# Performance work log

Hardware: AMD Instinct MI355X
Metric: run time of the kernel (lower is better)

## Reference

```python
import jax, jax.numpy as jnp
import numpy as np

J, C, F, K = 4096, 8192, 64, 2  # jobs, total nodes, out feats, TAGConv hops (DGL default K=2)


def setup_inputs() -> dict:
    key = jax.random.key(0)
    ks = jax.random.split(key, 8)
    h = jax.random.uniform(ks[0], (J,), jnp.float32)
    L = jax.random.uniform(ks[1], (J,), jnp.float32)
    W = jax.random.uniform(ks[2], (), jnp.float32)
    P = jax.random.uniform(ks[3], (), jnp.float32)
    N = jax.random.uniform(ks[4], (), jnp.float32)
    Graph = jax.random.randint(ks[5], (J, C), 0, 2).astype(jnp.float32)
    tag_w = jax.random.normal(ks[6], ((K + 1) * 6, F), jnp.float32) * 0.05  # TAGConv lin weight on concat of K+1 hops
    tag_b = jnp.zeros((F,), jnp.float32)
    lin_w = jax.random.normal(ks[7], (F, C), jnp.float32) * 0.05
    lin_b = jnp.zeros((C,), jnp.float32)
    return dict(h=h, L=L, W=W, P=P, N=N, Graph=Graph,
                tag_w=tag_w, tag_b=tag_b, lin_w=lin_w, lin_b=lin_b)


def _mask(Graph):
    Jn, Cn = Graph.shape
    row = Graph.sum(axis=1, keepdims=True)          # [J,1]
    col = Graph.sum(axis=0, keepdims=True)          # [1,C]
    colJ = col[:, :Jn]                               # [1,J]
    left = 1.0 - row - row.T - colJ - colJ.T         # [J,J]
    left = jnp.where(left == 1.0, 1.0, 0.0)
    left = jnp.triu(left, k=1)
    right = 1.0 - jnp.broadcast_to(row, (Jn, Cn - Jn))
    return jnp.concatenate([left, right], axis=1)    # [J,C]


def reference(h, L, W, P, N, Graph, tag_w, tag_b, lin_w, lin_b):
    Jn, Cn = Graph.shape
    # sort jobs by h descending, pair with L
    order = jnp.argsort(-h)
    jobList = jnp.stack([h[order], L[order]], axis=1)                 # [J,2]
    other = jnp.stack([W, P, N, jnp.asarray(1.0, h.dtype)])           # [4]
    X = jnp.concatenate([jobList, jnp.broadcast_to(other, (Jn, 4))], axis=1)  # [J,6]
    X = jnp.concatenate([X, jnp.zeros((Cn - Jn, 6), X.dtype)], axis=0)        # [C,6]
    # pad adjacency to square CxC
    A = jnp.concatenate([Graph, jnp.zeros((Cn - Jn, Cn), Graph.dtype)], axis=0)
    # DGL TAGConv: norm = clamp(in_deg,1)^-0.5; edge i->j iff A[i,j]==1 => aggregate = A^T @ x
    deg = A.sum(axis=0)
    norm = jnp.clip(deg, 1.0) ** -0.5

    def prop(x):
        return (A.T @ (x * norm[:, None])) * norm[:, None]

    f0 = X
    f1 = prop(f0)
    f2 = prop(f1)
    G_t = jnp.concatenate([f0, f1, f2], axis=1) @ tag_w + tag_b       # [C,F]
    Value = G_t[:Jn] @ lin_w + lin_b                                   # [J,C]
    tmp = Value - (1.0 - _mask(Graph)) * 10000.0
    Poss = jax.nn.softmax(tmp.reshape(-1)).reshape(tmp.shape)
    return (Value, Poss)
```

## Files before the change

kernel.cpp:

```cpp
#include <hip/hip_runtime.h>
#include <math.h>

#define JN 4096
#define CN 8192

typedef __attribute__((ext_vector_type(8))) short short8;
typedef __attribute__((ext_vector_type(4))) float f32x4;

#define WS_LWT    0
#define WS_ROWSUM 262144
#define WS_DEG    266240
#define WS_NORM   270336
#define WS_X      274432
#define WS_F1     299008
#define WS_F2     323584
#define WS_PART   348160

#define PS_BITR    0
#define PS_COLPART 524288
#define PS_P1      589824
#define PS_P2      983040

__device__ __forceinline__ unsigned short f2bf(float x) {
    unsigned int u = __float_as_uint(x);
    u += 0x7fffu + ((u >> 16) & 1u);
    return (unsigned short)(u >> 16);
}

__device__ __forceinline__ float gt_val(const float* __restrict__ x, const float* __restrict__ a,
                                        const float* __restrict__ b, const float* __restrict__ tw,
                                        float acc, int f) {
#pragma unroll
    for (int k = 0; k < 6; ++k) acc += x[k] * tw[k * 64 + f];
#pragma unroll
    for (int k = 0; k < 6; ++k) acc += a[k] * tw[(k + 6) * 64 + f];
#pragma unroll
    for (int k = 0; k < 6; ++k) acc += b[k] * tw[(k + 12) * 64 + f];
    return acc;
}

__global__ __launch_bounds__(256) void k_front(const float* __restrict__ G,
                                               const float* __restrict__ h, const float* __restrict__ L,
                                               const float* __restrict__ Wp, const float* __restrict__ Pp,
                                               const float* __restrict__ Np,
                                               float* __restrict__ rowsum,
                                               unsigned long long* __restrict__ bitR,
                                               float* __restrict__ X) {
    __shared__ float redf[4];
    __shared__ int redi[4];
    int wv = threadIdx.x >> 6, lane = threadIdx.x & 63;
    if (blockIdx.x < JN) {
        int row = blockIdx.x;
        const f32x4* g4 = (const f32x4*)(G + (size_t)row * CN);
        unsigned long long* brow = bitR + (size_t)row * 64;
        float s = 0.f;
#pragma unroll
        for (int i = 0; i < 4; ++i) {
            f32x4 v = __builtin_nontemporal_load(&g4[i * 256 + wv * 64 + lane]);
            s += v[0] + v[1] + v[2] + v[3];
            unsigned long long b0 = __ballot(v[0] != 0.f);
            unsigned long long b1 = __ballot(v[1] != 0.f);
            unsigned long long b2 = __ballot(v[2] != 0.f);
            unsigned long long b3 = __ballot(v[3] != 0.f);
            if (!lane) {
                int base = i * 16 + wv * 4;
                brow[base] = b0; brow[base + 1] = b1; brow[base + 2] = b2; brow[base + 3] = b3;
            }
        }
#pragma unroll
        for (int i = 4; i < 8; ++i) {
            f32x4 v = __builtin_nontemporal_load(&g4[i * 256 + wv * 64 + lane]);
            s += v[0] + v[1] + v[2] + v[3];
        }
        for (int o = 32; o; o >>= 1) s += __shfl_down(s, o, 64);
        if (!lane) redf[wv] = s;
        __syncthreads();
        if (!threadIdx.x) rowsum[row] = redf[0] + redf[1] + redf[2] + redf[3];
    } else {
        int i = blockIdx.x - JN;
        float hi = h[i];
        int cnt = 0;
        for (int j = threadIdx.x; j < JN; j += 256) {
            float hj = h[j];
            cnt += (hj > hi) || (hj == hi && j < i);
        }
        for (int o = 32; o; o >>= 1) cnt += __shfl_down(cnt, o, 64);
        if (!lane) redi[wv] = cnt;
        __syncthreads();
        if (!threadIdx.x) {
            int r = redi[0] + redi[1] + redi[2] + redi[3];
            float* xr = X + r * 6;
            xr[0] = hi; xr[1] = L[i]; xr[2] = *Wp; xr[3] = *Pp; xr[4] = *Np; xr[5] = 1.f;
        }
    }
}

__global__ __launch_bounds__(256) void k_colsum_bits(const unsigned long long* __restrict__ bitR,
                                                     float* __restrict__ colpart) {
    __shared__ unsigned long long s_bits[256][4];
    int bx = blockIdx.x, r0 = blockIdx.y * 256;
    int tid = threadIdx.x;
    for (int t = tid; t < 1024; t += 256) {
        int r = t >> 2, wl = t & 3;
        s_bits[r][wl] = bitR[(size_t)(r0 + r) * 64 + bx * 4 + wl];
    }
    __syncthreads();
    int wl = tid & 3, bit = tid >> 2;
    int cnt = 0;
    for (int r = 0; r < 256; ++r)
        cnt += (int)((s_bits[r][wl] >> bit) & 1ull);
    colpart[(size_t)blockIdx.y * JN + bx * 256 + tid] = (float)cnt;
}

__global__ __launch_bounds__(256) void k_normred(const float* __restrict__ colpart,
                                                 float* __restrict__ deg, float* __restrict__ norm) {
    int j = blockIdx.x * 256 + threadIdx.x;
    float d = 0.f;
    for (int ch = 0; ch < 16; ++ch) d += colpart[(size_t)ch * JN + j];
    deg[j] = d;
    float dc = d < 1.f ? 1.f : d;
    norm[j] = rsqrtf(dc);
}

__global__ __launch_bounds__(256) void k_prop1(const unsigned long long* __restrict__ bitR,
                                               const float* __restrict__ X, const float* __restrict__ norm,
                                               float* __restrict__ part) {
    __shared__ unsigned long long s_bits[256][4];
    __shared__ float s_in[256 * 6];
    int bx = blockIdx.x, r0 = blockIdx.y * 256;
    int tid = threadIdx.x;
    for (int t = tid; t < 1024; t += 256) {
        int r = t >> 2, wl = t & 3;
        s_bits[r][wl] = bitR[(size_t)(r0 + r) * 64 + bx * 4 + wl];
    }
    for (int t = tid; t < 1536; t += 256) {
        int row = r0 + t / 6;
        s_in[t] = X[r0 * 6 + t] * norm[row];
    }
    __syncthreads();
    int wl = tid & 3, bit = tid >> 2;
    float a0 = 0, a1 = 0, a2 = 0, a3 = 0, a4 = 0, a5 = 0;
    for (int r = 0; r < 256; ++r) {
        float g = (float)((s_bits[r][wl] >> bit) & 1ull);
        const float* x = &s_in[r * 6];
        a0 += g * x[0]; a1 += g * x[1]; a2 += g * x[2];
        a3 += g * x[3]; a4 += g * x[4]; a5 += g * x[5];
    }
    float* o = part + ((size_t)blockIdx.y * JN + bx * 256 + tid) * 6;
    o[0] = a0; o[1] = a1; o[2] = a2; o[3] = a3; o[4] = a4; o[5] = a5;
}

__global__ __launch_bounds__(256) void k_prop2(const unsigned long long* __restrict__ bitR,
                                               const float* __restrict__ p1, const float* __restrict__ norm,
                                               float* __restrict__ f1, float* __restrict__ part) {
    __shared__ unsigned long long s_bits[256][4];
    __shared__ float s_in[256 * 6];
    int bx = blockIdx.x, r0 = blockIdx.y * 256;
    int tid = threadIdx.x;
    for (int t = tid; t < 1024; t += 256) {
        int r = t >> 2, wl = t & 3;
        s_bits[r][wl] = bitR[(size_t)(r0 + r) * 64 + bx * 4 + wl];
    }
    for (int t = tid; t < 1536; t += 256) {
        float s = 0.f;
        for (int ch = 0; ch < 16; ++ch) s += p1[(size_t)ch * 24576 + r0 * 6 + t];
        int row = r0 + t / 6;
        float n = norm[row];
        float f1v = s * n;
        if (bx == 0) f1[r0 * 6 + t] = f1v;
        s_in[t] = f1v * n;
    }
    __syncthreads();
    int wl = tid & 3, bit = tid >> 2;
    float a0 = 0, a1 = 0, a2 = 0, a3 = 0, a4 = 0, a5 = 0;
    for (int r = 0; r < 256; ++r) {
        float g = (float)((s_bits[r][wl] >> bit) & 1ull);
        const float* x = &s_in[r * 6];
        a0 += g * x[0]; a1 += g * x[1]; a2 += g * x[2];
        a3 += g * x[3]; a4 += g * x[4]; a5 += g * x[5];
    }
    float* o = part + ((size_t)blockIdx.y * JN + bx * 256 + tid) * 6;
    o[0] = a0; o[1] = a1; o[2] = a2; o[3] = a3; o[4] = a4; o[5] = a5;
}

__global__ __launch_bounds__(256) void k_fin2(const float* __restrict__ p2, const float* __restrict__ norm,
                                              float* __restrict__ f2) {
    int idx = blockIdx.x * 256 + threadIdx.x;
    float s = 0.f;
    for (int ch = 0; ch < 16; ++ch) s += p2[(size_t)ch * 24576 + idx];
    f2[idx] = s * norm[idx / 6];
}

__global__ __launch_bounds__(256) void k_lwT(const float* __restrict__ lw, unsigned short* __restrict__ lwT) {
    __shared__ float s[64][65];
    int c0 = blockIdx.x * 64;
    for (int t = threadIdx.x; t < 4096; t += 256) {
        int f = t >> 6, cc = t & 63;
        s[f][cc] = lw[(size_t)f * CN + c0 + cc];
    }
    __syncthreads();
    for (int q = threadIdx.x; q < 512; q += 256) {
        int c = q >> 3, kc = q & 7;
        short8 pack;
#pragma unroll
        for (int i = 0; i < 8; ++i) pack[i] = (short)f2bf(s[kc * 8 + i][c]);
        *(short8*)(lwT + ((size_t)(c0 + c)) * 64 + kc * 8) = pack;
    }
}

#define GEMM_PROLOGUE()                                                                   \
    __shared__ unsigned short sGt[64 * 64];                                               \
    __shared__ unsigned short sW[256 * 64];                                               \
    __shared__ float s_tw[18 * 64];                                                       \
    __shared__ float s_tb[64];                                                            \
    int j0 = blockIdx.y * 64, c0 = blockIdx.x * 256, tid = threadIdx.x;                   \
    for (int t = tid; t < 1152; t += 256) s_tw[t] = tw[t];                                \
    if (tid < 64) s_tb[tid] = tb[tid];                                                    \
    for (int q = tid; q < 2048; q += 256) {                                               \
        int col = q >> 3, off = q & 7;                                                    \
        short8 v = *(const short8*)(lwT + ((size_t)(c0 + col)) * 64 + off * 8);           \
        int byte = (col * 128 + off * 16) ^ ((col & 7) << 4);                             \
        *(short8*)((char*)sW + byte) = v;                                                 \
    }                                                                                     \
    __syncthreads();                                                                      \
    {                                                                                     \
        int row = tid & 63, fg = tid >> 6;                                                \
        const float* xr = X + (size_t)(j0 + row) * 6;                                     \
        const float* ar = f1 + (size_t)(j0 + row) * 6;                                    \
        const float* br = f2 + (size_t)(j0 + row) * 6;                                    \
        float xv[6], av[6], bv[6];                                                        \
        for (int k = 0; k < 6; ++k) { xv[k] = xr[k]; av[k] = ar[k]; bv[k] = br[k]; }      \
        short8 p0, p1v;                                                                   \
        for (int i = 0; i < 16; ++i) {                                                    \
            int f = fg * 16 + i;                                                          \
            float acc = gt_val(xv, av, bv, s_tw, s_tb[f], f);                             \
            unsigned short u = f2bf(acc);                                                 \
            if (i < 8) p0[i] = (short)u; else p1v[i - 8] = (short)u;                      \
        }                                                                                 \
        int base = row * 128 + fg * 32;                                                   \
        *(short8*)((char*)sGt + (base ^ ((row & 7) << 4))) = p0;                          \
        *(short8*)((char*)sGt + ((base + 16) ^ ((row & 7) << 4))) = p1v;                  \
    }                                                                                     \
    __syncthreads();                                                                      \
    int lane = tid & 63, w = tid >> 6;                                                    \
    int lrow = lane & 15, kg = lane >> 4;                                                 \
    f32x4 acc[4][4];                                            \
    for (int m = 0; m < 4; ++m)                                                           \
        for (int n = 0; n < 4; ++n) acc[m][n] = (f32x4){0.f, 0.f, 0.f, 0.f};              \
    for (int ks = 0; ks < 2; ++ks) {                                                      \
        int kb = ks * 64 + kg * 16;                                                       \
        short8 wf[4], gf[4];                                                              \
        for (int m = 0; m < 4; ++m) {                                                     \
            int col = w * 64 + m * 16 + lrow;                                             \
            wf[m] = *(const short8*)((const char*)sW + ((col * 128 + kb) ^ ((col & 7) << 4))); \
        }                                                                                 \
        for (int n = 0; n < 4; ++n) {                                                     \
            int row = n * 16 + lrow;                                                      \
            gf[n] = *(const short8*)((const char*)sGt + ((row * 128 + kb) ^ ((row & 7) << 4))); \
        }                                                                                 \
        for (int m = 0; m < 4; ++m)                                                       \
            for (int n = 0; n < 4; ++n)                                                   \
                acc[m][n] = __builtin_amdgcn_mfma_f32_16x16x32_bf16(wf[m], gf[n], acc[m][n], 0, 0, 0); \
    }                                                                                     \
    bool left = (c0 < JN);                                                                \
    int cb[4]; f32x4 lb4[4], rsc4[4], dgc4[4];                                            \
    for (int m = 0; m < 4; ++m) {                                                         \
        cb[m] = c0 + w * 64 + m * 16 + kg * 4;                                            \
        lb4[m] = *(const f32x4*)&lb[cb[m]];                                               \
        if (left) { rsc4[m] = *(const f32x4*)&rowsum[cb[m]]; dgc4[m] = *(const f32x4*)&deg[cb[m]]; } \
        else      { rsc4[m] = (f32x4){0,0,0,0}; dgc4[m] = (f32x4){0,0,0,0}; }             \
    }

__global__ __launch_bounds__(256) void k_valueA(const float* __restrict__ X, const float* __restrict__ f1,
                                                const float* __restrict__ f2, const float* __restrict__ tw,
                                                const float* __restrict__ tb,
                                                const unsigned short* __restrict__ lwT,
                                                const float* __restrict__ lb,
                                                const float* __restrict__ rowsum, const float* __restrict__ deg,
                                                float* __restrict__ Value, float* __restrict__ partials) {
    GEMM_PROLOGUE()
    __shared__ float sRedM[4], sRedS[4];

    float mx = -INFINITY;
#pragma unroll
    for (int n = 0; n < 4; ++n) {
        int j = j0 + n * 16 + lrow;
        float rs_i = rowsum[j], dg_i = deg[j];
#pragma unroll
        for (int m = 0; m < 4; ++m) {
            f32x4 v4 = acc[m][n] + lb4[m];
            __builtin_nontemporal_store(v4, (f32x4*)&Value[(size_t)j * CN + cb[m]]);
            f32x4 t4;
#pragma unroll
            for (int u = 0; u < 4; ++u) {
                float om;
                if (left) {
                    bool m1 = ((rs_i + rsc4[m][u] + dg_i + dgc4[m][u]) == 0.0f) && (cb[m] + u > j);
                    om = m1 ? 0.f : 1.f;
                } else {
                    om = rs_i;
                }
                t4[u] = v4[u] - om * 10000.f;
            }
            acc[m][n] = t4;
            mx = fmaxf(fmaxf(fmaxf(mx, t4[0]), t4[1]), fmaxf(t4[2], t4[3]));
        }
    }
    float sm = 0.f;
#pragma unroll
    for (int n = 0; n < 4; ++n)
#pragma unroll
        for (int m = 0; m < 4; ++m)
#pragma unroll
            for (int u = 0; u < 4; ++u) sm += __expf(acc[m][n][u] - mx);

    for (int o = 32; o; o >>= 1) {
        float om_ = __shfl_down(mx, o, 64);
        float os_ = __shfl_down(sm, o, 64);
        float nm = fmaxf(mx, om_);
        sm = sm * __expf(mx - nm) + os_ * __expf(om_ - nm);
        mx = nm;
    }
    if (!lane) { sRedM[w] = mx; sRedS[w] = sm; }
    __syncthreads();
    if (!tid) {
        float M = sRedM[0], S = sRedS[0];
        for (int i = 1; i < 4; ++i) {
            float nm = fmaxf(M, sRedM[i]);
            S = S * __expf(M - nm) + sRedS[i] * __expf(sRedM[i] - nm);
            M = nm;
        }
        int bid = blockIdx.y * gridDim.x + blockIdx.x;
        partials[2 * bid] = M;
        partials[2 * bid + 1] = S;
    }
}

__global__ __launch_bounds__(256) void k_valueB(const float* __restrict__ X, const float* __restrict__ f1,
                                                const float* __restrict__ f2, const float* __restrict__ tw,
                                                const float* __restrict__ tb,
                                                const unsigned short* __restrict__ lwT,
                                                const float* __restrict__ lb,
                                                const float* __restrict__ rowsum, const float* __restrict__ deg,
                                                const float* __restrict__ partials, float* __restrict__ Poss) {
    __shared__ float sRedM[4], sRedS[4], sG[2];
    {
        int tid0 = threadIdx.x;
        float mx = -INFINITY, sm = 0.f;
        for (int i = tid0; i < 2048; i += 256) {
            float m = partials[2 * i], s = partials[2 * i + 1];
            float nm = fmaxf(mx, m);
            sm = sm * __expf(mx - nm) + s * __expf(m - nm);
            mx = nm;
        }
        for (int o = 32; o; o >>= 1) {
            float om_ = __shfl_down(mx, o, 64);
            float os_ = __shfl_down(sm, o, 64);
            float nm = fmaxf(mx, om_);
            sm = sm * __expf(mx - nm) + os_ * __expf(om_ - nm);
            mx = nm;
        }
        int lane0 = tid0 & 63, w0 = tid0 >> 6;
        if (!lane0) { sRedM[w0] = mx; sRedS[w0] = sm; }
        __syncthreads();
        if (!tid0) {
            float M = sRedM[0], S = sRedS[0];
            for (int i = 1; i < 4; ++i) {
                float nm = fmaxf(M, sRedM[i]);
                S = S * __expf(M - nm) + sRedS[i] * __expf(sRedM[i] - nm);
                M = nm;
            }
            sG[0] = M; sG[1] = S;
        }
        __syncthreads();
    }
    float gmax = sG[0];
    float ginv = 1.0f / sG[1];

    GEMM_PROLOGUE()
#pragma unroll
    for (int n = 0; n < 4; ++n) {
        int j = j0 + n * 16 + lrow;
        float rs_i = rowsum[j], dg_i = deg[j];
#pragma unroll
        for (int m = 0; m < 4; ++m) {
            f32x4 v4 = acc[m][n] + lb4[m];
            f32x4 o4;
#pragma unroll
            for (int u = 0; u < 4; ++u) {
                float om;
                if (left) {
                    bool m1 = ((rs_i + rsc4[m][u] + dg_i + dgc4[m][u]) == 0.0f) && (cb[m] + u > j);
                    om = m1 ? 0.f : 1.f;
                } else {
                    om = rs_i;
                }
                o4[u] = __expf(v4[u] - om * 10000.f - gmax) * ginv;
            }
            __builtin_nontemporal_store(o4, (f32x4*)&Poss[(size_t)j * CN + cb[m]]);
        }
    }
}

extern "C" void kernel_launch(void* const* d_in, const int* in_sizes, int n_in,
                              void* d_out, int out_size, void* d_ws, size_t ws_size,
                              hipStream_t stream) {
    const float* h  = (const float*)d_in[0];
    const float* L  = (const float*)d_in[1];
    const float* W  = (const float*)d_in[2];
    const float* P  = (const float*)d_in[3];
    const float* N  = (const float*)d_in[4];
    const float* G  = (const float*)d_in[5];
    const float* tw = (const float*)d_in[6];
    const float* tb = (const float*)d_in[7];
    const float* lw = (const float*)d_in[8];
    const float* lb = (const float*)d_in[9];

    float* ws = (float*)d_ws;
    unsigned short* lwT = (unsigned short*)(ws + WS_LWT);
    float* rowsum = ws + WS_ROWSUM;
    float* deg    = ws + WS_DEG;
    float* norm   = ws + WS_NORM;
    float* X      = ws + WS_X;
    float* f1     = ws + WS_F1;
    float* f2     = ws + WS_F2;
    float* part   = ws + WS_PART;

    float* Value = (float*)d_out;
    float* Poss  = Value + (size_t)JN * CN;

    unsigned long long* bitR = (unsigned long long*)(Poss + PS_BITR);
    float* colpart = Poss + PS_COLPART;
    float* p1      = Poss + PS_P1;
    float* p2      = Poss + PS_P2;

    k_lwT        <<<128, 256, 0, stream>>>(lw, lwT);
    k_front      <<<2 * JN, 256, 0, stream>>>(G, h, L, W, P, N, rowsum, bitR, X);
    k_colsum_bits<<<dim3(16, 16), 256, 0, stream>>>(bitR, colpart);
    k_normred    <<<16, 256, 0, stream>>>(colpart, deg, norm);
    k_prop1      <<<dim3(16, 16), 256, 0, stream>>>(bitR, X, norm, p1);
    k_prop2      <<<dim3(16, 16), 256, 0, stream>>>(bitR, p1, norm, f1, p2);
    k_fin2       <<<96, 256, 0, stream>>>(p2, norm, f2);
    k_valueA     <<<dim3(32, 64), 256, 0, stream>>>(X, f1, f2, tw, tb, lwT, lb, rowsum, deg, Value, part);
    k_valueB     <<<dim3(32, 64), 256, 0, stream>>>(X, f1, f2, tw, tb, lwT, lb, rowsum, deg, part, Poss);
}
```

Measured before the change: 184.5 us.

## Fold small kernels into neighbors and precompute bf16 G_t once

The lwT transpose is merged into k_front as extra blocks, and the degree/norm reduction is merged into k_prop1. k_fin2 is replaced by a k_gt kernel that computes the G_t projection once per row and stores it as bf16. The GEMM kernels then load this precomputed G_t instead of recomputing it in every block of both valueA and valueB. This removes two launches and a lot of redundant prologue math. The cost is redundant colpart reads across the prop1 blocks, plus an extra global round trip for Gtb.

```diff
diff --git a/kernel.cpp b/kernel.cpp
--- a/kernel.cpp
+++ b/kernel.cpp
@@ -8,13 +8,13 @@
 typedef __attribute__((ext_vector_type(4))) float f32x4;
 
 #define WS_LWT    0
-#define WS_ROWSUM 262144
-#define WS_DEG    266240
-#define WS_NORM   270336
-#define WS_X      274432
-#define WS_F1     299008
-#define WS_F2     323584
-#define WS_PART   348160
+#define WS_GTB    262144
+#define WS_ROWSUM 393216
+#define WS_DEG    397312
+#define WS_NORM   401408
+#define WS_X      405504
+#define WS_F1     430080
+#define WS_PART   454656
 
 #define PS_BITR    0
 #define PS_COLPART 524288
@@ -43,11 +43,14 @@
                                                const float* __restrict__ h, const float* __restrict__ L,
                                                const float* __restrict__ Wp, const float* __restrict__ Pp,
                                                const float* __restrict__ Np,
+                                               const float* __restrict__ lw,
                                                float* __restrict__ rowsum,
                                                unsigned long long* __restrict__ bitR,
-                                               float* __restrict__ X) {
+                                               float* __restrict__ X,
+                                               unsigned short* __restrict__ lwT) {
     __shared__ float redf[4];
     __shared__ int redi[4];
+    __shared__ float s_t[64][65];
     int wv = threadIdx.x >> 6, lane = threadIdx.x & 63;
     if (blockIdx.x < JN) {
         int row = blockIdx.x;
@@ -76,7 +79,7 @@
         if (!lane) redf[wv] = s;
         __syncthreads();
         if (!threadIdx.x) rowsum[row] = redf[0] + redf[1] + redf[2] + redf[3];
-    } else {
+    } else if (blockIdx.x < 2 * JN) {
         int i = blockIdx.x - JN;
         float hi = h[i];
         int cnt = 0;
@@ -91,6 +94,20 @@
             int r = redi[0] + redi[1] + redi[2] + redi[3];
             float* xr = X + r * 6;
             xr[0] = hi; xr[1] = L[i]; xr[2] = *Wp; xr[3] = *Pp; xr[4] = *Np; xr[5] = 1.f;
+        }
+    } else {
+        int c0 = (blockIdx.x - 2 * JN) * 64;
+        for (int t = threadIdx.x; t < 4096; t += 256) {
+            int f = t >> 6, cc = t & 63;
+            s_t[f][cc] = lw[(size_t)f * CN + c0 + cc];
+        }
+        __syncthreads();
+        for (int q = threadIdx.x; q < 512; q += 256) {
+            int c = q >> 3, kc = q & 7;
+            short8 pack;
+#pragma unroll
+            for (int i = 0; i < 8; ++i) pack[i] = (short)f2bf(s_t[kc * 8 + i][c]);
+            *(short8*)(lwT + ((size_t)(c0 + c)) * 64 + kc * 8) = pack;
         }
     }
 }
@@ -112,31 +129,31 @@
     colpart[(size_t)blockIdx.y * JN + bx * 256 + tid] = (float)cnt;
 }
 
-__global__ __launch_bounds__(256) void k_normred(const float* __restrict__ colpart,
-                                                 float* __restrict__ deg, float* __restrict__ norm) {
-    int j = blockIdx.x * 256 + threadIdx.x;
-    float d = 0.f;
-    for (int ch = 0; ch < 16; ++ch) d += colpart[(size_t)ch * JN + j];
-    deg[j] = d;
-    float dc = d < 1.f ? 1.f : d;
-    norm[j] = rsqrtf(dc);
-}
-
 __global__ __launch_bounds__(256) void k_prop1(const unsigned long long* __restrict__ bitR,
-                                               const float* __restrict__ X, const float* __restrict__ norm,
+                                               const float* __restrict__ X,
+                                               const float* __restrict__ colpart,
+                                               float* __restrict__ deg, float* __restrict__ norm,
                                                float* __restrict__ part) {
     __shared__ unsigned long long s_bits[256][4];
     __shared__ float s_in[256 * 6];
+    __shared__ float s_norm[256];
     int bx = blockIdx.x, r0 = blockIdx.y * 256;
     int tid = threadIdx.x;
+    {
+        float d = 0.f;
+        for (int ch = 0; ch < 16; ++ch) d += colpart[(size_t)ch * JN + r0 + tid];
+        float dc = d < 1.f ? 1.f : d;
+        float nv = rsqrtf(dc);
+        s_norm[tid] = nv;
+        if (bx == 0) { deg[r0 + tid] = d; norm[r0 + tid] = nv; }
+    }
     for (int t = tid; t < 1024; t += 256) {
         int r = t >> 2, wl = t & 3;
         s_bits[r][wl] = bitR[(size_t)(r0 + r) * 64 + bx * 4 + wl];
     }
-    for (int t = tid; t < 1536; t += 256) {
-        int row = r0 + t / 6;
-        s_in[t] = X[r0 * 6 + t] * norm[row];
-    }
+    __syncthreads();
+    for (int t = tid; t < 1536; t += 256)
+        s_in[t] = X[r0 * 6 + t] * s_norm[t / 6];
     __syncthreads();
     int wl = tid & 3, bit = tid >> 2;
     float a0 = 0, a1 = 0, a2 = 0, a3 = 0, a4 = 0, a5 = 0;
@@ -183,63 +200,56 @@
     o[0] = a0; o[1] = a1; o[2] = a2; o[3] = a3; o[4] = a4; o[5] = a5;
 }
 
-__global__ __launch_bounds__(256) void k_fin2(const float* __restrict__ p2, const float* __restrict__ norm,
-                                              float* __restrict__ f2) {
-    int idx = blockIdx.x * 256 + threadIdx.x;
-    float s = 0.f;
-    for (int ch = 0; ch < 16; ++ch) s += p2[(size_t)ch * 24576 + idx];
-    f2[idx] = s * norm[idx / 6];
-}
-
-__global__ __launch_bounds__(256) void k_lwT(const float* __restrict__ lw, unsigned short* __restrict__ lwT) {
-    __shared__ float s[64][65];
-    int c0 = blockIdx.x * 64;
-    for (int t = threadIdx.x; t < 4096; t += 256) {
-        int f = t >> 6, cc = t & 63;
-        s[f][cc] = lw[(size_t)f * CN + c0 + cc];
-    }
-    __syncthreads();
-    for (int q = threadIdx.x; q < 512; q += 256) {
-        int c = q >> 3, kc = q & 7;
-        short8 pack;
-#pragma unroll
-        for (int i = 0; i < 8; ++i) pack[i] = (short)f2bf(s[kc * 8 + i][c]);
-        *(short8*)(lwT + ((size_t)(c0 + c)) * 64 + kc * 8) = pack;
-    }
+__global__ __launch_bounds__(256) void k_gt(const float* __restrict__ p2, const float* __restrict__ norm,
+                                            const float* __restrict__ f1, const float* __restrict__ X,
+                                            const float* __restrict__ tw, const float* __restrict__ tb,
+                                            unsigned short* __restrict__ Gtb) {
+    __shared__ float s_x[64 * 6], s_f1[64 * 6], s_f2[64 * 6];
+    __shared__ float s_tw[18 * 64], s_tb[64];
+    int j0 = blockIdx.x * 64, tid = threadIdx.x;
+    for (int t = tid; t < 1152; t += 256) s_tw[t] = tw[t];
+    if (tid < 64) s_tb[tid] = tb[tid];
+    for (int t = tid; t < 384; t += 256) {
+        s_x[t] = X[j0 * 6 + t];
+        s_f1[t] = f1[j0 * 6 + t];
+        float s = 0.f;
+        for (int ch = 0; ch < 16; ++ch) s += p2[(size_t)ch * 24576 + j0 * 6 + t];
+        s_f2[t] = s * norm[j0 + t / 6];
+    }
+    __syncthreads();
+    int row = tid & 63, fg = tid >> 6;
+    float xv[6], av[6], bv[6];
+#pragma unroll
+    for (int k = 0; k < 6; ++k) {
+        xv[k] = s_x[row * 6 + k]; av[k] = s_f1[row * 6 + k]; bv[k] = s_f2[row * 6 + k];
+    }
+    short8 p0, p1v;
+#pragma unroll
+    for (int i = 0; i < 16; ++i) {
+        int f = fg * 16 + i;
+        float acc = gt_val(xv, av, bv, s_tw, s_tb[f], f);
+        unsigned short u = f2bf(acc);
+        if (i < 8) p0[i] = (short)u; else p1v[i - 8] = (short)u;
+    }
+    *(short8*)(Gtb + (size_t)(j0 + row) * 64 + fg * 16) = p0;
+    *(short8*)(Gtb + (size_t)(j0 + row) * 64 + fg * 16 + 8) = p1v;
 }
 
 #define GEMM_PROLOGUE()                                                                   \
     __shared__ unsigned short sGt[64 * 64];                                               \
     __shared__ unsigned short sW[256 * 64];                                               \
-    __shared__ float s_tw[18 * 64];                                                       \
-    __shared__ float s_tb[64];                                                            \
     int j0 = blockIdx.y * 64, c0 = blockIdx.x * 256, tid = threadIdx.x;                   \
-    for (int t = tid; t < 1152; t += 256) s_tw[t] = tw[t];                                \
-    if (tid < 64) s_tb[tid] = tb[tid];                                                    \
     for (int q = tid; q < 2048; q += 256) {                                               \
         int col = q >> 3, off = q & 7;                                                    \
         short8 v = *(const short8*)(lwT + ((size_t)(c0 + col)) * 64 + off * 8);           \
         int byte = (col * 128 + off * 16) ^ ((col & 7) << 4);                             \
         *(short8*)((char*)sW + byte) = v;                                                 \
     }                                                                                     \
-    __syncthreads();                                                                      \
-    {                                                                                     \
-        int row = tid & 63, fg = tid >> 6;                                                \
-        const float* xr = X + (size_t)(j0 + row) * 6;                                     \
-        const float* ar = f1 + (size_t)(j0 + row) * 6;                                    \
-        const float* br = f2 + (size_t)(j0 + row) * 6;                                    \
-        float xv[6], av[6], bv[6];                                                        \
-        for (int k = 0; k < 6; ++k) { xv[k] = xr[k]; av[k] = ar[k]; bv[k] = br[k]; }      \
-        short8 p0, p1v;                                                                   \
-        for (int i = 0; i < 16; ++i) {                                                    \
-            int f = fg * 16 + i;                                                          \
-            float acc = gt_val(xv, av, bv, s_tw, s_tb[f], f);                             \
-            unsigned short u = f2bf(acc);                                                 \
-            if (i < 8) p0[i] = (short)u; else p1v[i - 8] = (short)u;                      \
-        }                                                                                 \
-        int base = row * 128 + fg * 32;                                                   \
-        *(short8*)((char*)sGt + (base ^ ((row & 7) << 4))) = p0;                          \
-        *(short8*)((char*)sGt + ((base + 16) ^ ((row & 7) << 4))) = p1v;                  \
+    for (int q = tid; q < 512; q += 256) {                                                \
+        int row = q >> 3, off = q & 7;                                                    \
+        short8 v = *(const short8*)(Gtb + ((size_t)(j0 + row)) * 64 + off * 8);           \
+        int byte = (row * 128 + off * 16) ^ ((row & 7) << 4);                             \
+        *(short8*)((char*)sGt + byte) = v;                                                \
     }                                                                                     \
     __syncthreads();                                                                      \
     int lane = tid & 63, w = tid >> 6;                                                    \
@@ -271,9 +281,7 @@
         else      { rsc4[m] = (f32x4){0,0,0,0}; dgc4[m] = (f32x4){0,0,0,0}; }             \
     }
 
-__global__ __launch_bounds__(256) void k_valueA(const float* __restrict__ X, const float* __restrict__ f1,
-                                                const float* __restrict__ f2, const float* __restrict__ tw,
-                                                const float* __restrict__ tb,
+__global__ __launch_bounds__(256) void k_valueA(const unsigned short* __restrict__ Gtb,
                                                 const unsigned short* __restrict__ lwT,
                                                 const float* __restrict__ lb,
                                                 const float* __restrict__ rowsum, const float* __restrict__ deg,
@@ -336,9 +344,7 @@
     }
 }
 
-__global__ __launch_bounds__(256) void k_valueB(const float* __restrict__ X, const float* __restrict__ f1,
-                                                const float* __restrict__ f2, const float* __restrict__ tw,
-                                                const float* __restrict__ tb,
+__global__ __launch_bounds__(256) void k_valueB(const unsigned short* __restrict__ Gtb,
                                                 const unsigned short* __restrict__ lwT,
                                                 const float* __restrict__ lb,
                                                 const float* __restrict__ rowsum, const float* __restrict__ deg,
@@ -418,12 +424,12 @@
 
     float* ws = (float*)d_ws;
     unsigned short* lwT = (unsigned short*)(ws + WS_LWT);
+    unsigned short* Gtb = (unsigned short*)(ws + WS_GTB);
     float* rowsum = ws + WS_ROWSUM;
     float* deg    = ws + WS_DEG;
     float* norm   = ws + WS_NORM;
     float* X      = ws + WS_X;
     float* f1     = ws + WS_F1;
-    float* f2     = ws + WS_F2;
     float* part   = ws + WS_PART;
 
     float* Value = (float*)d_out;
@@ -434,13 +440,11 @@
     float* p1      = Poss + PS_P1;
     float* p2      = Poss + PS_P2;
 
-    k_lwT        <<<128, 256, 0, stream>>>(lw, lwT);
-    k_front      <<<2 * JN, 256, 0, stream>>>(G, h, L, W, P, N, rowsum, bitR, X);
+    k_front      <<<2 * JN + 128, 256, 0, stream>>>(G, h, L, W, P, N, lw, rowsum, bitR, X, lwT);
     k_colsum_bits<<<dim3(16, 16), 256, 0, stream>>>(bitR, colpart);
-    k_normred    <<<16, 256, 0, stream>>>(colpart, deg, norm);
-    k_prop1      <<<dim3(16, 16), 256, 0, stream>>>(bitR, X, norm, p1);
+    k_prop1      <<<dim3(16, 16), 256, 0, stream>>>(bitR, X, colpart, deg, norm, p1);
     k_prop2      <<<dim3(16, 16), 256, 0, stream>>>(bitR, p1, norm, f1, p2);
-    k_fin2       <<<96, 256, 0, stream>>>(p2, norm, f2);
-    k_valueA     <<<dim3(32, 64), 256, 0, stream>>>(X, f1, f2, tw, tb, lwT, lb, rowsum, deg, Value, part);
-    k_valueB     <<<dim3(32, 64), 256, 0, stream>>>(X, f1, f2, tw, tb, lwT, lb, rowsum, deg, part, Poss);
-}
+    k_gt         <<<64, 256, 0, stream>>>(p2, norm, f1, X, tw, tb, Gtb);
+    k_valueA     <<<dim3(32, 64), 256, 0, stream>>>(Gtb, lwT, lb, rowsum, deg, Value, part);
+    k_valueB     <<<dim3(32, 64), 256, 0, stream>>>(Gtb, lwT, lb, rowsum, deg, part, Poss);
+}
```

New measurement: 149.9 us. 18.7% less time.
